# Kernel tuning notes

Measured on AMD Instinct MI355X. Metric: run time of the kernel, lower is better.

The kernel has to match this reference:

```python
import jax, jax.numpy as jnp
import numpy as np

N_NODES = 50000
N_EDGES = 800000
IN_C = 16
HID_C = 16
OUT_C = 10
N_GRAPHS = 500
EDGE_DIM = 3
MLP_HID = 25
BN_EPS = 1e-5


def setup_inputs() -> dict:
    key = jax.random.key(0)
    ks = iter(jax.random.split(key, 40))

    def nrm(shape, scale=1.0):
        return jax.random.normal(next(ks), shape, dtype=jnp.float32) * scale

    inp = {}
    inp["x"] = nrm((N_NODES, IN_C))
    inp["edge_index"] = jax.random.randint(next(ks), (2, N_EDGES), 0, N_NODES, dtype=jnp.int32)
    inp["edge_attr"] = jax.random.uniform(next(ks), (N_EDGES, EDGE_DIM), dtype=jnp.float32)
    inp["batch"] = jnp.sort(jax.random.randint(next(ks), (N_NODES,), 0, N_GRAPHS, dtype=jnp.int32))

    def bn_params():
        g = jax.random.uniform(next(ks), (MLP_HID,), minval=0.8, maxval=1.2, dtype=jnp.float32)
        b = nrm((MLP_HID,), 0.1)
        mu = nrm((MLP_HID,), 0.1)
        var = jax.random.uniform(next(ks), (MLP_HID,), minval=0.5, maxval=1.5, dtype=jnp.float32)
        return g, b, mu, var

    # edge MLP 1: 3 -> 25 -> IN_C*HID_C
    inp["W1a"] = nrm((EDGE_DIM, MLP_HID), 0.3)
    inp["b1a"] = nrm((MLP_HID,), 0.05)
    inp["g1"], inp["bt1"], inp["m1"], inp["v1"] = bn_params()
    inp["W1b"] = nrm((MLP_HID, IN_C * HID_C), 0.1)
    inp["b1b"] = nrm((IN_C * HID_C,), 0.05)
    inp["root1"] = nrm((IN_C, HID_C), 0.2)
    inp["bias1"] = nrm((HID_C,), 0.05)

    # edge MLP 2: 3 -> 25 -> HID_C*HID_C
    inp["W2a"] = nrm((EDGE_DIM, MLP_HID), 0.3)
    inp["b2a"] = nrm((MLP_HID,), 0.05)
    inp["g2"], inp["bt2"], inp["m2"], inp["v2"] = bn_params()
    inp["W2b"] = nrm((MLP_HID, HID_C * HID_C), 0.1)
    inp["b2b"] = nrm((HID_C * HID_C,), 0.05)
    inp["root2"] = nrm((HID_C, HID_C), 0.2)
    inp["bias2"] = nrm((HID_C,), 0.05)

    # final MLP([HID_C, OUT_C]) -> single plain linear (plain_last)
    inp["fcW"] = nrm((HID_C, OUT_C), 0.2)
    inp["fcb"] = nrm((OUT_C,), 0.05)
    return inp


def _edge_mlp(e, Wa, ba, g, bt, mu, var, Wb, bb):
    # Linear -> BatchNorm(eval) -> ReLU -> (dropout=eval identity) -> Linear
    h = e @ Wa + ba
    h = g * (h - mu) * jax.lax.rsqrt(var + BN_EPS) + bt
    h = jax.nn.relu(h)
    return h @ Wb + bb


def _nnconv(x, src, dst, w_edge, root, bias, out_dim):
    # message: x_j [E,in] times per-edge weight [E,in,out]
    msg = jnp.einsum("ei,eio->eo", x[src], w_edge)
    agg = jax.ops.segment_sum(msg, dst, num_segments=N_NODES)
    deg = jax.ops.segment_sum(jnp.ones((src.shape[0],), msg.dtype), dst, num_segments=N_NODES)
    agg = agg / jnp.maximum(deg, 1.0)[:, None]  # mean aggregation
    return agg + x @ root + bias


def reference(x, edge_index, edge_attr, batch,
              W1a, b1a, g1, bt1, m1, v1, W1b, b1b, root1, bias1,
              W2a, b2a, g2, bt2, m2, v2, W2b, b2b, root2, bias2,
              fcW, fcb):
    src, dst = edge_index[0], edge_index[1]

    w1 = _edge_mlp(edge_attr, W1a, b1a, g1, bt1, m1, v1, W1b, b1b).reshape(-1, IN_C, HID_C)
    x = jax.nn.elu(_nnconv(x, src, dst, w1, root1, bias1, HID_C))

    w2 = _edge_mlp(edge_attr, W2a, b2a, g2, bt2, m2, v2, W2b, b2b).reshape(-1, HID_C, HID_C)
    x = jax.nn.elu(_nnconv(x, src, dst, w2, root2, bias2, HID_C))

    # global mean pooling over graphs
    pooled = jax.ops.segment_sum(x, batch, num_segments=N_GRAPHS)
    cnt = jax.ops.segment_sum(jnp.ones((x.shape[0],), x.dtype), batch, num_segments=N_GRAPHS)
    pooled = pooled / jnp.maximum(cnt, 1.0)[:, None]

    return pooled @ fcW + fcb  # [N_GRAPHS, OUT_C]
```

## Files before the change

kernel.cpp:

```cpp
#include <hip/hip_runtime.h>
#include <math.h>

#define N_NODES 50000
#define N_EDGES 800000
#define IN_C 16
#define HID_C 16
#define OUT_C 10
#define N_GRAPHS 500
#define EDGE_DIM 3
#define MLP_HID 25
#define BN_EPS 1e-5f

#define SCAN_NB ((N_NODES + 255) / 256)

typedef __attribute__((ext_vector_type(8))) short short8;
typedef __attribute__((ext_vector_type(4))) float f32x4;
typedef __attribute__((ext_vector_type(2))) float f32x2;
union U4S8 { uint4 u; short8 s; };


__global__ __launch_bounds__(256) void setup_kernel(
    const float* __restrict__ W1a, const float* __restrict__ b1a,
    const float* __restrict__ g1, const float* __restrict__ bt1,
    const float* __restrict__ m1, const float* __restrict__ v1,
    const float* __restrict__ W2a, const float* __restrict__ b2a,
    const float* __restrict__ g2, const float* __restrict__ bt2,
    const float* __restrict__ m2, const float* __restrict__ v2,
    const float* __restrict__ W1b, const float* __restrict__ b1b,
    const float* __restrict__ W2b, const float* __restrict__ b2b,
    const int* __restrict__ batch,
    float* __restrict__ AC1, float* __restrict__ AC2,
    unsigned int* __restrict__ WHI1, unsigned int* __restrict__ WHI2,
    int* __restrict__ goff)
{
    const int blk = blockIdx.x;
    const int tid = threadIdx.x;
    if (blk < 7) {
        int t = blk * 256 + tid;
        if (t >= 1664) return;
        const float *Wb, *bb; unsigned int *WH;
        int tl = t;
        if (t < 832) { Wb = W1b; bb = b1b; WH = WHI1; }
        else { tl = t - 832; Wb = W2b; bb = b2b; WH = WHI2; }
        int m = tl >> 6;
        int L = tl & 63;
        int q = L >> 4, o = L & 15;
        unsigned int hi[8];
        for (int j = 0; j < 8; ++j) {
            int kp = m*32 + q*8 + j;
            int k = kp >> 4, i = kp & 15;
            float w = (k < 25) ? Wb[k*256 + i*16 + o] : bb[i*16 + o];
            unsigned int u = __float_as_uint(w);
            hi[j] = (u + 0x7FFFu + ((u >> 16) & 1u)) >> 16;
        }
        int base = (m*64 + L) * 4;
        for (int d = 0; d < 4; ++d)
            WH[base + d] = hi[2*d] | (hi[2*d+1] << 16);
        return;
    }
    if (blk == 7) {
        if (tid < 26) {
            int k = tid;
            if (k < 25) {
                float sc = g1[k] / sqrtf(v1[k] + BN_EPS);
                AC1[k*4+0] = sc * W1a[0*MLP_HID+k];
                AC1[k*4+1] = sc * W1a[1*MLP_HID+k];
                AC1[k*4+2] = sc * W1a[2*MLP_HID+k];
                AC1[k*4+3] = sc * (b1a[k] - m1[k]) + bt1[k];
            } else {
                AC1[100] = 0.f; AC1[101] = 0.f; AC1[102] = 0.f; AC1[103] = 1.f;
            }
        } else if (tid >= 32 && tid < 58) {
            int k = tid - 32;
            if (k < 25) {
                float sc = g2[k] / sqrtf(v2[k] + BN_EPS);
                AC2[k*4+0] = sc * W2a[0*MLP_HID+k];
                AC2[k*4+1] = sc * W2a[1*MLP_HID+k];
                AC2[k*4+2] = sc * W2a[2*MLP_HID+k];
                AC2[k*4+3] = sc * (b2a[k] - m2[k]) + bt2[k];
            } else {
                AC2[100] = 0.f; AC2[101] = 0.f; AC2[102] = 0.f; AC2[103] = 1.f;
            }
        }
    }
    int g = (blk - 7) * 256 + tid;
    if (g <= N_GRAPHS) {
        int lo = 0, hi = N_NODES;
        while (lo < hi) {
            int mid = (lo + hi) >> 1;
            if (batch[mid] < g) lo = mid + 1; else hi = mid;
        }
        goff[g] = lo;
    }
}


__global__ __launch_bounds__(256) void rank_kernel(const int* __restrict__ dst,
                                                   int* __restrict__ cnt,
                                                   int* __restrict__ rank) {
    int e = blockIdx.x * blockDim.x + threadIdx.x;
    if (e < N_EDGES) rank[e] = atomicAdd(&cnt[dst[e]], 1);
}

__global__ __launch_bounds__(256) void scan_p1(const int* __restrict__ cnt,
                                               int* __restrict__ bsum) {
    __shared__ int lds[256];
    int t = threadIdx.x;
    int idx = blockIdx.x * 256 + t;
    lds[t] = (idx < N_NODES) ? cnt[idx] : 0;
    __syncthreads();
    for (int d = 128; d > 0; d >>= 1) {
        if (t < d) lds[t] += lds[t + d];
        __syncthreads();
    }
    if (t == 0) bsum[blockIdx.x] = lds[0];
}

__global__ __launch_bounds__(256) void scan_p2(const int* __restrict__ bsum,
                                               int* __restrict__ bpre,
                                               int* __restrict__ off) {
    __shared__ int lds[256];
    int t = threadIdx.x;
    lds[t] = (t < SCAN_NB) ? bsum[t] : 0;
    __syncthreads();
    for (int d = 1; d < 256; d <<= 1) {
        int v = (t >= d) ? lds[t - d] : 0;
        __syncthreads();
        lds[t] += v;
        __syncthreads();
    }
    if (t < SCAN_NB) bpre[t] = (t > 0) ? lds[t - 1] : 0;
    if (t == 255) off[N_NODES] = lds[255];
}

__global__ __launch_bounds__(256) void scan_p3(const int* __restrict__ cnt,
                                               const int* __restrict__ bpre,
                                               int* __restrict__ off) {
    __shared__ int lds[256];
    int t = threadIdx.x;
    int idx = blockIdx.x * 256 + t;
    int v = (idx < N_NODES) ? cnt[idx] : 0;
    lds[t] = v;
    __syncthreads();
    for (int d = 1; d < 256; d <<= 1) {
        int u = (t >= d) ? lds[t - d] : 0;
        __syncthreads();
        lds[t] += u;
        __syncthreads();
    }
    if (idx < N_NODES) off[idx] = bpre[blockIdx.x] + lds[t] - v;
}

__global__ __launch_bounds__(256) void pos2_kernel(const int* __restrict__ dst,
                                                   const int* __restrict__ off,
                                                   int* __restrict__ rank) {
    int e = blockIdx.x * blockDim.x + threadIdx.x;
    if (e < N_EDGES) rank[e] = off[dst[e]] + rank[e];
}


__device__ __forceinline__ U4S8 packH(float h, float4 xl, float4 xh) {
    f32x2 h2; h2.x = h; h2.y = h;
    f32x2 m0; m0.x = xl.x; m0.y = xl.y; m0 *= h2;
    f32x2 m1; m1.x = xl.z; m1.y = xl.w; m1 *= h2;
    f32x2 m2; m2.x = xh.x; m2.y = xh.y; m2 *= h2;
    f32x2 m3; m3.x = xh.z; m3.y = xh.w; m3 *= h2;
    U4S8 r;
    r.u.x = __builtin_amdgcn_perm(__float_as_uint(m0.y), __float_as_uint(m0.x), 0x07060302u);
    r.u.y = __builtin_amdgcn_perm(__float_as_uint(m1.y), __float_as_uint(m1.x), 0x07060302u);
    r.u.z = __builtin_amdgcn_perm(__float_as_uint(m2.y), __float_as_uint(m2.x), 0x07060302u);
    r.u.w = __builtin_amdgcn_perm(__float_as_uint(m3.y), __float_as_uint(m3.x), 0x07060302u);
    return r;
}

__global__ __launch_bounds__(256) void edge_mfma4_kernel(
    const float* __restrict__ xin,
    const int* __restrict__ src,
    const int* __restrict__ P,
    const float* __restrict__ eattr,
    const float* __restrict__ AC,
    const unsigned int* __restrict__ WHI,
    float* __restrict__ msg_buf)
{
    const int tid  = threadIdx.x;
    const int wave = tid >> 6;
    const int lane = tid & 63;
    const int q    = lane >> 4;
    const int el   = lane & 15;
    const int i0   = (q & 1) * 8;
    const bool bsel = (q >> 1) != 0;
    const int E0   = (blockIdx.x * 4 + wave) * 32;
    const int eA   = E0 + el;
    const int eB   = E0 + 16 + el;

    const int sA = src[eA], sB = src[eB];
    const float aA0 = eattr[(size_t)eA*3+0];
    const float aA1 = eattr[(size_t)eA*3+1];
    const float aA2 = eattr[(size_t)eA*3+2];
    const float aB0 = eattr[(size_t)eB*3+0];
    const float aB1 = eattr[(size_t)eB*3+1];
    const float aB2 = eattr[(size_t)eB*3+2];
    const uint4 ppA = *(const uint4*)(P + E0 + q*4);
    const uint4 ppB = *(const uint4*)(P + E0 + 16 + q*4);
    const float4* xpA = (const float4*)(xin + (size_t)sA*16 + i0);
    const float4 xlA = xpA[0], xhA = xpA[1];
    const float4* xpB = (const float4*)(xin + (size_t)sB*16 + i0);
    const float4 xlB = xpB[0], xhB = xpB[1];

    f32x4 accA = {0.f, 0.f, 0.f, 0.f};
    f32x4 accB = {0.f, 0.f, 0.f, 0.f};
    #pragma unroll 1
    for (int m = 0; m < 13; ++m) {
        const float4 Ae = *(const float4*)(AC + m*8);
        const float4 Ao = *(const float4*)(AC + m*8 + 4);
        U4S8 w; w.u = ((const uint4*)WHI)[m*64 + lane];
        float hAe = fmaxf(fmaf(aA2, Ae.z, fmaf(aA1, Ae.y, fmaf(aA0, Ae.x, Ae.w))), 0.f);
        float hAo = fmaxf(fmaf(aA2, Ao.z, fmaf(aA1, Ao.y, fmaf(aA0, Ao.x, Ao.w))), 0.f);
        float hA  = bsel ? hAo : hAe;
        float hBe = fmaxf(fmaf(aB2, Ae.z, fmaf(aB1, Ae.y, fmaf(aB0, Ae.x, Ae.w))), 0.f);
        float hBo = fmaxf(fmaf(aB2, Ao.z, fmaf(aB1, Ao.y, fmaf(aB0, Ao.x, Ao.w))), 0.f);
        float hB  = bsel ? hBo : hBe;
        U4S8 hfA = packH(hA, xlA, xhA);
        U4S8 hfB = packH(hB, xlB, xhB);
        accA = __builtin_amdgcn_mfma_f32_16x16x32_bf16(hfA.s, w.s, accA, 0, 0, 0);
        accB = __builtin_amdgcn_mfma_f32_16x16x32_bf16(hfB.s, w.s, accB, 0, 0, 0);
    }

    msg_buf[(size_t)((unsigned)ppA.x) * HID_C + el] = accA[0];
    msg_buf[(size_t)((unsigned)ppA.y) * HID_C + el] = accA[1];
    msg_buf[(size_t)((unsigned)ppA.z) * HID_C + el] = accA[2];
    msg_buf[(size_t)((unsigned)ppA.w) * HID_C + el] = accA[3];
    msg_buf[(size_t)((unsigned)ppB.x) * HID_C + el] = accB[0];
    msg_buf[(size_t)((unsigned)ppB.y) * HID_C + el] = accB[1];
    msg_buf[(size_t)((unsigned)ppB.z) * HID_C + el] = accB[2];
    msg_buf[(size_t)((unsigned)ppB.w) * HID_C + el] = accB[3];
}

__global__ __launch_bounds__(256) void node_gather_kernel(
    const float* __restrict__ xin, const float* __restrict__ msg_buf,
    const int* __restrict__ off,
    const float* __restrict__ root, const float* __restrict__ bias,
    float* __restrict__ xout)
{
    int t = blockIdx.x * blockDim.x + threadIdx.x;
    int n = t >> 4;
    int o = t & 15;
    if (n >= N_NODES) return;
    int lo = off[n], hi = off[n+1];
    float inv = 1.f / fmaxf((float)(hi - lo), 1.f);

    float s0 = 0.f, s1 = 0.f, s2 = 0.f, s3 = 0.f;
    int r = lo;
    for (; r + 4 <= hi; r += 4) {
        s0 += msg_buf[(size_t)r     * HID_C + o];
        s1 += msg_buf[(size_t)(r+1) * HID_C + o];
        s2 += msg_buf[(size_t)(r+2) * HID_C + o];
        s3 += msg_buf[(size_t)(r+3) * HID_C + o];
    }
    for (; r < hi; ++r) s0 += msg_buf[(size_t)r * HID_C + o];
    float s = (s0 + s1) + (s2 + s3);

    float acc = fmaf(s, inv, bias[o]);
    const float* xr = xin + (size_t)n * IN_C;
    #pragma unroll
    for (int i = 0; i < IN_C; ++i)
        acc = fmaf(xr[i], root[i*HID_C+o], acc);
    xout[(size_t)n*HID_C + o] = acc > 0.f ? acc : (expf(acc) - 1.f);
}

__global__ __launch_bounds__(64) void pool_final_kernel(
    const float* __restrict__ xin, const int* __restrict__ goff,
    const float* __restrict__ fcW, const float* __restrict__ fcb,
    float* __restrict__ out)
{
    __shared__ float part[4][HID_C];
    __shared__ float pooled[HID_C];
    int g = blockIdx.x;
    int t = threadIdx.x;
    int c = t & 15, sub = t >> 4;
    int lo = goff[g], hi = goff[g+1];
    float s = 0.f;
    for (int n = lo + sub; n < hi; n += 4)
        s += xin[(size_t)n*HID_C + c];
    part[sub][c] = s;
    __syncthreads();
    if (t < HID_C) {
        pooled[t] = (part[0][t] + part[1][t] + part[2][t] + part[3][t])
                    / fmaxf((float)(hi - lo), 1.f);
    }
    __syncthreads();
    if (t < OUT_C) {
        float acc = fcb[t];
        #pragma unroll
        for (int i = 0; i < HID_C; ++i)
            acc = fmaf(pooled[i], fcW[i*OUT_C+t], acc);
        out[g*OUT_C + t] = acc;
    }
}


extern "C" void kernel_launch(void* const* d_in, const int* in_sizes, int n_in,
                              void* d_out, int out_size, void* d_ws, size_t ws_size,
                              hipStream_t stream)
{
    const float* x     = (const float*)d_in[0];
    const int*   ei    = (const int*)d_in[1];
    const float* eattr = (const float*)d_in[2];
    const int*   batch = (const int*)d_in[3];
    const float* W1a   = (const float*)d_in[4];
    const float* b1a   = (const float*)d_in[5];
    const float* g1    = (const float*)d_in[6];
    const float* bt1   = (const float*)d_in[7];
    const float* m1    = (const float*)d_in[8];
    const float* v1    = (const float*)d_in[9];
    const float* W1b   = (const float*)d_in[10];
    const float* b1b   = (const float*)d_in[11];
    const float* root1 = (const float*)d_in[12];
    const float* bias1 = (const float*)d_in[13];
    const float* W2a   = (const float*)d_in[14];
    const float* b2a   = (const float*)d_in[15];
    const float* g2    = (const float*)d_in[16];
    const float* bt2   = (const float*)d_in[17];
    const float* m2    = (const float*)d_in[18];
    const float* v2    = (const float*)d_in[19];
    const float* W2b   = (const float*)d_in[20];
    const float* b2b   = (const float*)d_in[21];
    const float* root2 = (const float*)d_in[22];
    const float* bias2 = (const float*)d_in[23];
    const float* fcW   = (const float*)d_in[24];
    const float* fcb   = (const float*)d_in[25];

    const int* src = ei;
    const int* dst = ei + N_EDGES;

    float* ws   = (float*)d_ws;
    float* MSG  = ws;
    float* X1   = ws + 12800000;
    float* X2   = ws + 13600000;
    int*   RANK = (int*)(ws + 14400000);
    int*   CNT  = (int*)(ws + 15200000);
    int*   OFF  = (int*)(ws + 15250000);
    int*   GOFF = (int*)(ws + 15300064);
    unsigned int* WHI1 = (unsigned int*)(ws + 15300576);
    unsigned int* WHI2 = (unsigned int*)(ws + 15303904);
    float* AC1  = ws + 15307232;
    float* AC2  = ws + 15307344;
    int*   BSUM = (int*)(ws + 15307456);
    int*   BPRE = (int*)(ws + 15307712);

    hipMemsetAsync(CNT, 0, N_NODES * sizeof(int), stream);
    setup_kernel<<<9, 256, 0, stream>>>(W1a, b1a, g1, bt1, m1, v1,
                                        W2a, b2a, g2, bt2, m2, v2,
                                        W1b, b1b, W2b, b2b, batch,
                                        AC1, AC2, WHI1, WHI2, GOFF);
    rank_kernel<<<N_EDGES/256, 256, 0, stream>>>(dst, CNT, RANK);
    scan_p1<<<SCAN_NB, 256, 0, stream>>>(CNT, BSUM);
    scan_p2<<<1, 256, 0, stream>>>(BSUM, BPRE, OFF);
    scan_p3<<<SCAN_NB, 256, 0, stream>>>(CNT, BPRE, OFF);
    pos2_kernel<<<N_EDGES/256, 256, 0, stream>>>(dst, OFF, RANK);

    edge_mfma4_kernel<<<N_EDGES/128, 256, 0, stream>>>(x, src, RANK, eattr,
                                                       AC1, WHI1, MSG);
    node_gather_kernel<<<(N_NODES*16+255)/256, 256, 0, stream>>>(x, MSG, OFF,
                                                                 root1, bias1, X1);

    edge_mfma4_kernel<<<N_EDGES/128, 256, 0, stream>>>(X1, src, RANK, eattr,
                                                       AC2, WHI2, MSG);
    node_gather_kernel<<<(N_NODES*16+255)/256, 256, 0, stream>>>(X1, MSG, OFF,
                                                                 root2, bias2, X2);

    pool_final_kernel<<<N_GRAPHS, 64, 0, stream>>>(X2, GOFF, fcW, fcb, (float*)d_out);
}
```

Measured before the change: 277.7 us.

## Fold memset and scan stages into fewer kernels, switch edge MFMA to fp16

```diff
diff --git a/kernel.cpp b/kernel.cpp
--- a/kernel.cpp
+++ b/kernel.cpp
@@ -13,10 +13,11 @@
 
 #define SCAN_NB ((N_NODES + 255) / 256)
 
-typedef __attribute__((ext_vector_type(8))) short short8;
+typedef __attribute__((ext_vector_type(8))) _Float16 half8;
+typedef __attribute__((ext_vector_type(2))) _Float16 half2v;
 typedef __attribute__((ext_vector_type(4))) float f32x4;
-typedef __attribute__((ext_vector_type(2))) float f32x2;
-union U4S8 { uint4 u; short8 s; };
+union U4H8 { uint4 u; half8 h; half2v p[4]; };
+union HU { _Float16 h; unsigned short u; };
 
 
 __global__ __launch_bounds__(256) void setup_kernel(
@@ -30,8 +31,8 @@
     const float* __restrict__ W2b, const float* __restrict__ b2b,
     const int* __restrict__ batch,
     float* __restrict__ AC1, float* __restrict__ AC2,
-    unsigned int* __restrict__ WHI1, unsigned int* __restrict__ WHI2,
-    int* __restrict__ goff)
+    unsigned int* __restrict__ WF1, unsigned int* __restrict__ WF2,
+    int* __restrict__ goff, int* __restrict__ cnt, int* __restrict__ ticket)
 {
     const int blk = blockIdx.x;
     const int tid = threadIdx.x;
@@ -40,8 +41,8 @@
         if (t >= 1664) return;
         const float *Wb, *bb; unsigned int *WH;
         int tl = t;
-        if (t < 832) { Wb = W1b; bb = b1b; WH = WHI1; }
-        else { tl = t - 832; Wb = W2b; bb = b2b; WH = WHI2; }
+        if (t < 832) { Wb = W1b; bb = b1b; WH = WF1; }
+        else { tl = t - 832; Wb = W2b; bb = b2b; WH = WF2; }
         int m = tl >> 6;
         int L = tl & 63;
         int q = L >> 4, o = L & 15;
@@ -50,48 +51,54 @@
             int kp = m*32 + q*8 + j;
             int k = kp >> 4, i = kp & 15;
             float w = (k < 25) ? Wb[k*256 + i*16 + o] : bb[i*16 + o];
-            unsigned int u = __float_as_uint(w);
-            hi[j] = (u + 0x7FFFu + ((u >> 16) & 1u)) >> 16;
+            HU cv; cv.h = (_Float16)w;
+            hi[j] = cv.u;
         }
         int base = (m*64 + L) * 4;
         for (int d = 0; d < 4; ++d)
             WH[base + d] = hi[2*d] | (hi[2*d+1] << 16);
         return;
     }
-    if (blk == 7) {
-        if (tid < 26) {
-            int k = tid;
-            if (k < 25) {
-                float sc = g1[k] / sqrtf(v1[k] + BN_EPS);
-                AC1[k*4+0] = sc * W1a[0*MLP_HID+k];
-                AC1[k*4+1] = sc * W1a[1*MLP_HID+k];
-                AC1[k*4+2] = sc * W1a[2*MLP_HID+k];
-                AC1[k*4+3] = sc * (b1a[k] - m1[k]) + bt1[k];
-            } else {
-                AC1[100] = 0.f; AC1[101] = 0.f; AC1[102] = 0.f; AC1[103] = 1.f;
+    if (blk == 7 || blk == 8) {
+        if (blk == 7) {
+            if (tid < 26) {
+                int k = tid;
+                if (k < 25) {
+                    float sc = g1[k] / sqrtf(v1[k] + BN_EPS);
+                    AC1[k*4+0] = sc * W1a[0*MLP_HID+k];
+                    AC1[k*4+1] = sc * W1a[1*MLP_HID+k];
+                    AC1[k*4+2] = sc * W1a[2*MLP_HID+k];
+                    AC1[k*4+3] = sc * (b1a[k] - m1[k]) + bt1[k];
+                } else {
+                    AC1[100] = 0.f; AC1[101] = 0.f; AC1[102] = 0.f; AC1[103] = 1.f;
+                }
+            } else if (tid >= 32 && tid < 58) {
+                int k = tid - 32;
+                if (k < 25) {
+                    float sc = g2[k] / sqrtf(v2[k] + BN_EPS);
+                    AC2[k*4+0] = sc * W2a[0*MLP_HID+k];
+                    AC2[k*4+1] = sc * W2a[1*MLP_HID+k];
+                    AC2[k*4+2] = sc * W2a[2*MLP_HID+k];
+                    AC2[k*4+3] = sc * (b2a[k] - m2[k]) + bt2[k];
+                } else {
+                    AC2[100] = 0.f; AC2[101] = 0.f; AC2[102] = 0.f; AC2[103] = 1.f;
+                }
             }
-        } else if (tid >= 32 && tid < 58) {
-            int k = tid - 32;
-            if (k < 25) {
-                float sc = g2[k] / sqrtf(v2[k] + BN_EPS);
-                AC2[k*4+0] = sc * W2a[0*MLP_HID+k];
-                AC2[k*4+1] = sc * W2a[1*MLP_HID+k];
-                AC2[k*4+2] = sc * W2a[2*MLP_HID+k];
-                AC2[k*4+3] = sc * (b2a[k] - m2[k]) + bt2[k];
-            } else {
-                AC2[100] = 0.f; AC2[101] = 0.f; AC2[102] = 0.f; AC2[103] = 1.f;
+        }
+        int g = (blk - 7) * 256 + tid;
+        if (g <= N_GRAPHS) {
+            int lo = 0, hi = N_NODES;
+            while (lo < hi) {
+                int mid = (lo + hi) >> 1;
+                if (batch[mid] < g) lo = mid + 1; else hi = mid;
             }
-        }
-    }
-    int g = (blk - 7) * 256 + tid;
-    if (g <= N_GRAPHS) {
-        int lo = 0, hi = N_NODES;
-        while (lo < hi) {
-            int mid = (lo + hi) >> 1;
-            if (batch[mid] < g) lo = mid + 1; else hi = mid;
-        }
-        goff[g] = lo;
-    }
+            goff[g] = lo;
+        }
+        return;
+    }
+    int idx = (blk - 9) * 256 + tid;
+    if (idx < N_NODES) cnt[idx] = 0;
+    if (blk == 9 && tid == 0) *ticket = 0;
 }
 
 
@@ -103,8 +110,12 @@
 }
 
 __global__ __launch_bounds__(256) void scan_p1(const int* __restrict__ cnt,
-                                               int* __restrict__ bsum) {
+                                               int* __restrict__ bsum,
+                                               int* __restrict__ bpre,
+                                               int* __restrict__ off,
+                                               int* __restrict__ ticket) {
     __shared__ int lds[256];
+    __shared__ int sDone;
     int t = threadIdx.x;
     int idx = blockIdx.x * 256 + t;
     lds[t] = (idx < N_NODES) ? cnt[idx] : 0;
@@ -113,20 +124,22 @@
         if (t < d) lds[t] += lds[t + d];
         __syncthreads();
     }
-    if (t == 0) bsum[blockIdx.x] = lds[0];
-}
-
-__global__ __launch_bounds__(256) void scan_p2(const int* __restrict__ bsum,
-                                               int* __restrict__ bpre,
-                                               int* __restrict__ off) {
-    __shared__ int lds[256];
-    int t = threadIdx.x;
-    lds[t] = (t < SCAN_NB) ? bsum[t] : 0;
+    if (t == 0) {
+        bsum[blockIdx.x] = lds[0];
+        __threadfence();
+        sDone = atomicAdd(ticket, 1);
+    }
+    __syncthreads();
+    if (sDone != SCAN_NB - 1) return;
+    __threadfence();
+    int v = (t < SCAN_NB) ? bsum[t] : 0;
+    __syncthreads();
+    lds[t] = v;
     __syncthreads();
     for (int d = 1; d < 256; d <<= 1) {
-        int v = (t >= d) ? lds[t - d] : 0;
-        __syncthreads();
-        lds[t] += v;
+        int u = (t >= d) ? lds[t - d] : 0;
+        __syncthreads();
+        lds[t] += u;
         __syncthreads();
     }
     if (t < SCAN_NB) bpre[t] = (t > 0) ? lds[t - 1] : 0;
@@ -151,35 +164,16 @@
     if (idx < N_NODES) off[idx] = bpre[blockIdx.x] + lds[t] - v;
 }
 
-__global__ __launch_bounds__(256) void pos2_kernel(const int* __restrict__ dst,
-                                                   const int* __restrict__ off,
-                                                   int* __restrict__ rank) {
-    int e = blockIdx.x * blockDim.x + threadIdx.x;
-    if (e < N_EDGES) rank[e] = off[dst[e]] + rank[e];
-}
-
-
-__device__ __forceinline__ U4S8 packH(float h, float4 xl, float4 xh) {
-    f32x2 h2; h2.x = h; h2.y = h;
-    f32x2 m0; m0.x = xl.x; m0.y = xl.y; m0 *= h2;
-    f32x2 m1; m1.x = xl.z; m1.y = xl.w; m1 *= h2;
-    f32x2 m2; m2.x = xh.x; m2.y = xh.y; m2 *= h2;
-    f32x2 m3; m3.x = xh.z; m3.y = xh.w; m3 *= h2;
-    U4S8 r;
-    r.u.x = __builtin_amdgcn_perm(__float_as_uint(m0.y), __float_as_uint(m0.x), 0x07060302u);
-    r.u.y = __builtin_amdgcn_perm(__float_as_uint(m1.y), __float_as_uint(m1.x), 0x07060302u);
-    r.u.z = __builtin_amdgcn_perm(__float_as_uint(m2.y), __float_as_uint(m2.x), 0x07060302u);
-    r.u.w = __builtin_amdgcn_perm(__float_as_uint(m3.y), __float_as_uint(m3.x), 0x07060302u);
-    return r;
-}
-
-__global__ __launch_bounds__(256) void edge_mfma4_kernel(
+
+__global__ __launch_bounds__(256) void edge_mfma5_kernel(
     const float* __restrict__ xin,
     const int* __restrict__ src,
-    const int* __restrict__ P,
+    const int* __restrict__ dst,
+    const int* __restrict__ rank,
+    const int* __restrict__ off,
     const float* __restrict__ eattr,
     const float* __restrict__ AC,
-    const unsigned int* __restrict__ WHI,
+    const unsigned int* __restrict__ WF,
     float* __restrict__ msg_buf)
 {
     const int tid  = threadIdx.x;
@@ -194,18 +188,30 @@
     const int eB   = E0 + 16 + el;
 
     const int sA = src[eA], sB = src[eB];
+    const int pA = off[dst[eA]] + rank[eA];
+    const int pB = off[dst[eB]] + rank[eB];
     const float aA0 = eattr[(size_t)eA*3+0];
     const float aA1 = eattr[(size_t)eA*3+1];
     const float aA2 = eattr[(size_t)eA*3+2];
     const float aB0 = eattr[(size_t)eB*3+0];
     const float aB1 = eattr[(size_t)eB*3+1];
     const float aB2 = eattr[(size_t)eB*3+2];
-    const uint4 ppA = *(const uint4*)(P + E0 + q*4);
-    const uint4 ppB = *(const uint4*)(P + E0 + 16 + q*4);
     const float4* xpA = (const float4*)(xin + (size_t)sA*16 + i0);
     const float4 xlA = xpA[0], xhA = xpA[1];
     const float4* xpB = (const float4*)(xin + (size_t)sB*16 + i0);
     const float4 xlB = xpB[0], xhB = xpB[1];
+
+    U4H8 xA, xB;
+    {
+        const float x8A[8] = {xlA.x,xlA.y,xlA.z,xlA.w,xhA.x,xhA.y,xhA.z,xhA.w};
+        const float x8B[8] = {xlB.x,xlB.y,xlB.z,xlB.w,xhB.x,xhB.y,xhB.z,xhB.w};
+        #pragma unroll
+        for (int j = 0; j < 4; ++j) {
+            half2v ta; ta.x = (_Float16)x8A[2*j]; ta.y = (_Float16)x8A[2*j+1];
+            half2v tb; tb.x = (_Float16)x8B[2*j]; tb.y = (_Float16)x8B[2*j+1];
+            xA.p[j] = ta; xB.p[j] = tb;
+        }
+    }
 
     f32x4 accA = {0.f, 0.f, 0.f, 0.f};
     f32x4 accB = {0.f, 0.f, 0.f, 0.f};
@@ -213,27 +219,33 @@
     for (int m = 0; m < 13; ++m) {
         const float4 Ae = *(const float4*)(AC + m*8);
         const float4 Ao = *(const float4*)(AC + m*8 + 4);
-        U4S8 w; w.u = ((const uint4*)WHI)[m*64 + lane];
-        float hAe = fmaxf(fmaf(aA2, Ae.z, fmaf(aA1, Ae.y, fmaf(aA0, Ae.x, Ae.w))), 0.f);
-        float hAo = fmaxf(fmaf(aA2, Ao.z, fmaf(aA1, Ao.y, fmaf(aA0, Ao.x, Ao.w))), 0.f);
-        float hA  = bsel ? hAo : hAe;
-        float hBe = fmaxf(fmaf(aB2, Ae.z, fmaf(aB1, Ae.y, fmaf(aB0, Ae.x, Ae.w))), 0.f);
-        float hBo = fmaxf(fmaf(aB2, Ao.z, fmaf(aB1, Ao.y, fmaf(aB0, Ao.x, Ao.w))), 0.f);
-        float hB  = bsel ? hBo : hBe;
-        U4S8 hfA = packH(hA, xlA, xhA);
-        U4S8 hfB = packH(hB, xlB, xhB);
-        accA = __builtin_amdgcn_mfma_f32_16x16x32_bf16(hfA.s, w.s, accA, 0, 0, 0);
-        accB = __builtin_amdgcn_mfma_f32_16x16x32_bf16(hfB.s, w.s, accB, 0, 0, 0);
-    }
-
-    msg_buf[(size_t)((unsigned)ppA.x) * HID_C + el] = accA[0];
-    msg_buf[(size_t)((unsigned)ppA.y) * HID_C + el] = accA[1];
-    msg_buf[(size_t)((unsigned)ppA.z) * HID_C + el] = accA[2];
-    msg_buf[(size_t)((unsigned)ppA.w) * HID_C + el] = accA[3];
-    msg_buf[(size_t)((unsigned)ppB.x) * HID_C + el] = accB[0];
-    msg_buf[(size_t)((unsigned)ppB.y) * HID_C + el] = accB[1];
-    msg_buf[(size_t)((unsigned)ppB.z) * HID_C + el] = accB[2];
-    msg_buf[(size_t)((unsigned)ppB.w) * HID_C + el] = accB[3];
+        const float A0 = bsel ? Ao.x : Ae.x;
+        const float A1 = bsel ? Ao.y : Ae.y;
+        const float A2 = bsel ? Ao.z : Ae.z;
+        const float A3 = bsel ? Ao.w : Ae.w;
+        U4H8 w; w.u = ((const uint4*)WF)[m*64 + lane];
+        float hA = fmaxf(fmaf(aA2, A2, fmaf(aA1, A1, fmaf(aA0, A0, A3))), 0.f);
+        float hB = fmaxf(fmaf(aB2, A2, fmaf(aB1, A1, fmaf(aB0, A0, A3))), 0.f);
+        _Float16 ha = (_Float16)hA, hb = (_Float16)hB;
+        half2v hA2; hA2.x = ha; hA2.y = ha;
+        half2v hB2; hB2.x = hb; hB2.y = hb;
+        U4H8 fA, fB;
+        #pragma unroll
+        for (int j = 0; j < 4; ++j) {
+            fA.p[j] = hA2 * xA.p[j];
+            fB.p[j] = hB2 * xB.p[j];
+        }
+        accA = __builtin_amdgcn_mfma_f32_16x16x32_f16(fA.h, w.h, accA, 0, 0, 0);
+        accB = __builtin_amdgcn_mfma_f32_16x16x32_f16(fB.h, w.h, accB, 0, 0, 0);
+    }
+
+    #pragma unroll
+    for (int r = 0; r < 4; ++r) {
+        int rowA = __shfl(pA, q*4 + r);
+        int rowB = __shfl(pB, q*4 + r);
+        msg_buf[(size_t)rowA * HID_C + el] = accA[r];
+        msg_buf[(size_t)rowB * HID_C + el] = accB[r];
+    }
 }
 
 __global__ __launch_bounds__(256) void node_gather_kernel(
@@ -341,31 +353,28 @@
     int*   CNT  = (int*)(ws + 15200000);
     int*   OFF  = (int*)(ws + 15250000);
     int*   GOFF = (int*)(ws + 15300064);
-    unsigned int* WHI1 = (unsigned int*)(ws + 15300576);
-    unsigned int* WHI2 = (unsigned int*)(ws + 15303904);
+    unsigned int* WF1 = (unsigned int*)(ws + 15300576);
+    unsigned int* WF2 = (unsigned int*)(ws + 15303904);
     float* AC1  = ws + 15307232;
     float* AC2  = ws + 15307344;
     int*   BSUM = (int*)(ws + 15307456);
     int*   BPRE = (int*)(ws + 15307712);
-
-    hipMemsetAsync(CNT, 0, N_NODES * sizeof(int), stream);
-    setup_kernel<<<9, 256, 0, stream>>>(W1a, b1a, g1, bt1, m1, v1,
-                                        W2a, b2a, g2, bt2, m2, v2,
-                                        W1b, b1b, W2b, b2b, batch,
-                                        AC1, AC2, WHI1, WHI2, GOFF);
+    int*   TICK = (int*)(ws + 15307968);
+
+    setup_kernel<<<9 + SCAN_NB, 256, 0, stream>>>(
+        W1a, b1a, g1, bt1, m1, v1, W2a, b2a, g2, bt2, m2, v2,
+        W1b, b1b, W2b, b2b, batch, AC1, AC2, WF1, WF2, GOFF, CNT, TICK);
     rank_kernel<<<N_EDGES/256, 256, 0, stream>>>(dst, CNT, RANK);
-    scan_p1<<<SCAN_NB, 256, 0, stream>>>(CNT, BSUM);
-    scan_p2<<<1, 256, 0, stream>>>(BSUM, BPRE, OFF);
+    scan_p1<<<SCAN_NB, 256, 0, stream>>>(CNT, BSUM, BPRE, OFF, TICK);
     scan_p3<<<SCAN_NB, 256, 0, stream>>>(CNT, BPRE, OFF);
-    pos2_kernel<<<N_EDGES/256, 256, 0, stream>>>(dst, OFF, RANK);
-
-    edge_mfma4_kernel<<<N_EDGES/128, 256, 0, stream>>>(x, src, RANK, eattr,
-                                                       AC1, WHI1, MSG);
+
+    edge_mfma5_kernel<<<N_EDGES/128, 256, 0, stream>>>(x, src, dst, RANK, OFF,
+                                                       eattr, AC1, WF1, MSG);
     node_gather_kernel<<<(N_NODES*16+255)/256, 256, 0, stream>>>(x, MSG, OFF,
                                                                  root1, bias1, X1);
 
-    edge_mfma4_kernel<<<N_EDGES/128, 256, 0, stream>>>(X1, src, RANK, eattr,
-                                                       AC2, WHI2, MSG);
+    edge_mfma5_kernel<<<N_EDGES/128, 256, 0, stream>>>(X1, src, dst, RANK, OFF,
+                                                       eattr, AC2, WF2, MSG);
     node_gather_kernel<<<(N_NODES*16+255)/256, 256, 0, stream>>>(X1, MSG, OFF,
                                                                  root2, bias2, X2);
 
```

Result: faster. 269.7 us (-2.9%).
